# Kernel tuning notes

Hardware: AMD Instinct MI355X
Metric: run time of the kernel (lower is better)

The kernel has to match this reference:

```python
import jax, jax.numpy as jnp
import numpy as np

B, S, HID = 2, 2048, 2048
H, KV, D, E = 16, 4, 128, 32
NB = 9  # num_behavior + 1
EPS = 1e-6
SCALING = (E + D) ** -0.5


def rmsnorm(x, w, eps=EPS):
    # normalize over last dim in fp32, like Qwen3MoeRMSNorm
    xf = x.astype(jnp.float32)
    var = jnp.mean(xf * xf, axis=-1, keepdims=True)
    return (xf * jax.lax.rsqrt(var + eps)).astype(x.dtype) * w


def setup_inputs() -> dict:
    key = jax.random.key(0)
    ks = jax.random.split(key, 12)
    s = lambda n: 1.0 / np.sqrt(n)
    return {
        "hidden_states": jax.random.normal(ks[0], (B, S, HID), jnp.float32),
        "behavior_index": jax.random.randint(ks[1], (B, S), 0, NB),
        "q_proj_w": jax.random.normal(ks[2], (H * D, HID), jnp.float32) * s(HID),
        "k_proj_w": jax.random.normal(ks[3], (KV * D, HID), jnp.float32) * s(HID),
        "v_proj_w": jax.random.normal(ks[4], (KV * D, HID), jnp.float32) * s(HID),
        "o_proj_w": jax.random.normal(ks[5], (HID, H * D), jnp.float32) * s(H * D),
        "q_norm_w": jnp.ones((D,), jnp.float32),
        "k_norm_w": jnp.ones((D,), jnp.float32),
        "qbe_table": jax.random.normal(ks[6], (NB, H * E), jnp.float32),
        "kbe_table": jax.random.normal(ks[7], (NB, KV * E), jnp.float32),
        "qbn_w": jnp.ones((E,), jnp.float32),
        "kbn_w": jnp.ones((E,), jnp.float32),
    }


def reference(hidden_states, behavior_index, q_proj_w, k_proj_w, v_proj_w,
              o_proj_w, q_norm_w, k_norm_w, qbe_table, kbe_table, qbn_w, kbn_w):
    b, s, _ = hidden_states.shape
    # QKV projections + per-head RMSNorm on q/k
    q = rmsnorm((hidden_states @ q_proj_w.T).reshape(b, s, H, D), q_norm_w)
    k = rmsnorm((hidden_states @ k_proj_w.T).reshape(b, s, KV, D), k_norm_w)
    v = (hidden_states @ v_proj_w.T).reshape(b, s, KV, D)
    q = q.transpose(0, 2, 1, 3)  # [b,H,s,D]
    k = k.transpose(0, 2, 1, 3)  # [b,KV,s,D]
    v = v.transpose(0, 2, 1, 3)  # [b,KV,s,D]
    # behavior embeddings: lookup -> per-head RMSNorm -> concat onto head_dim
    qbe = rmsnorm(qbe_table[behavior_index].reshape(b, s, H, E), qbn_w).transpose(0, 2, 1, 3)
    kbe = rmsnorm(kbe_table[behavior_index].reshape(b, s, KV, E), kbn_w).transpose(0, 2, 1, 3)
    q = jnp.concatenate([q, qbe], axis=-1)  # [b,H,s,D+E]
    k = jnp.concatenate([k, kbe], axis=-1)  # [b,KV,s,D+E]
    # GQA: repeat kv heads
    g = H // KV
    k = jnp.repeat(k, g, axis=1)
    v = jnp.repeat(v, g, axis=1)
    # eager attention, causal, softmax in fp32
    scores = jnp.einsum('bhqd,bhkd->bhqk', q, k) * SCALING
    causal = jnp.tril(jnp.ones((s, s), bool))
    scores = jnp.where(causal, scores, jnp.finfo(scores.dtype).min)
    attn = jax.nn.softmax(scores.astype(jnp.float32), axis=-1).astype(q.dtype)
    out = jnp.einsum('bhqk,bhkd->bhqd', attn, v)  # [b,H,s,D]
    out = out.transpose(0, 2, 1, 3).reshape(b, s, H * D)
    return out @ o_proj_w.T
```

## Files before the change

### kernel.cpp

```cpp
#include <hip/hip_runtime.h>

typedef unsigned short u16;
typedef unsigned int u32;
typedef __bf16 bf16x8 __attribute__((ext_vector_type(8)));
typedef __bf16 b16x4 __attribute__((ext_vector_type(4)));
typedef short s16x4 __attribute__((ext_vector_type(4)));
typedef float f32x4 __attribute__((ext_vector_type(4)));

#define SCALE 0.07905694150420949f

__device__ __forceinline__ float bf2f(u16 h) { return __uint_as_float(((u32)h) << 16); }
__device__ __forceinline__ u16 f2bf(float f) {
  u32 u = __float_as_uint(f);
  u += 0x7fffu + ((u >> 16) & 1u);
  return (u16)(u >> 16);
}
__device__ __forceinline__ u16 f2bf_fast(float f) {
  return (u16)((__float_as_uint(f) + 0x8000u) >> 16);
}
__device__ __forceinline__ bf16x8 ldfrag(const u16* p) {
  int4 t = *reinterpret_cast<const int4*>(p);
  return __builtin_bit_cast(bf16x8, t);
}

__device__ __forceinline__ f32x4 mfma16x16(s16x4 a, s16x4 b, f32x4 c) {
#if __has_builtin(__builtin_amdgcn_mfma_f32_16x16x16bf16_1k)
  return __builtin_amdgcn_mfma_f32_16x16x16bf16_1k(a, b, c, 0, 0, 0);
#elif __has_builtin(__builtin_amdgcn_mfma_f32_16x16x16_bf16)
  return __builtin_amdgcn_mfma_f32_16x16x16_bf16(__builtin_bit_cast(b16x4, a),
                                                 __builtin_bit_cast(b16x4, b), c, 0, 0, 0);
#else
  asm volatile("s_nop 2\n\tv_mfma_f32_16x16x16_bf16 %0, %1, %2, %0"
               : "+v"(c) : "v"(a), "v"(b));
  return c;
#endif
}

__device__ __forceinline__ void gld16(const u16* g, u16* l) {
  __builtin_amdgcn_global_load_lds((const __attribute__((address_space(1))) u32*)(const void*)g,
                                   (__attribute__((address_space(3))) u32*)(void*)l, 16, 0, 0);
}

__global__ void conv_f32_bf16(const float* __restrict__ in, u16* __restrict__ out, int n) {
  int n4 = n >> 2;
  for (int i = blockIdx.x * blockDim.x + threadIdx.x; i < n4; i += gridDim.x * blockDim.x) {
    float4 v = reinterpret_cast<const float4*>(in)[i];
    ushort4 o = {f2bf(v.x), f2bf(v.y), f2bf(v.z), f2bf(v.w)};
    reinterpret_cast<ushort4*>(out)[i] = o;
  }
}

template <int OUT_BF16>
__global__ __launch_bounds__(256, 2) void gemm_bt(const u16* __restrict__ A,
                                                  const u16* __restrict__ Bw,
                                                  void* __restrict__ Cv,
                                                  int M, int N, int K) {
  __shared__ __align__(16) u16 As[2][8192];
  __shared__ __align__(16) u16 Bs[2][8192];
  const int tid = threadIdx.x;
  const int nbn = N >> 7;
  const int cpx = gridDim.x >> 3;
  const int swz = (blockIdx.x & 7) * cpx + (blockIdx.x >> 3);
  const int bm = swz / nbn, bn = swz % nbn;
  const int row0 = bm << 7, col0 = bn << 7;
  const int lane = tid & 63, w = tid >> 6;
  const int lg = lane >> 4, lr = lane & 15;
  const int wr = w >> 1, wc = w & 1;
  const int nt = K >> 6;

  auto stage = [&](int slot, int t) {
    const size_t k0 = (size_t)t << 6;
#pragma unroll
    for (int it = 0; it < 4; ++it) {
      int G = it * 256 + tid;
      int r = G >> 3, p = G & 7;
      int gs = p ^ (r & 7);
      gld16(&A[(size_t)(row0 + r) * K + k0 + gs * 8], &As[slot][(size_t)G * 8]);
      gld16(&Bw[(size_t)(col0 + r) * K + k0 + gs * 8], &Bs[slot][(size_t)G * 8]);
    }
  };

  f32x4 acc[4][4] = {};
  stage(0, 0);
  __syncthreads();

  for (int t = 0; t < nt; ++t) {
    const int slot = t & 1;
    if (t + 1 < nt) stage(slot ^ 1, t + 1);
#pragma unroll
    for (int kk = 0; kk < 2; ++kk) {
      bf16x8 af[4], bv[4];
#pragma unroll
      for (int m = 0; m < 4; ++m) {
        int r = wr * 64 + m * 16 + lr;
        int g = (kk * 4 + lg) ^ (lr & 7);
        af[m] = ldfrag(&As[slot][r * 64 + g * 8]);
      }
#pragma unroll
      for (int n = 0; n < 4; ++n) {
        int r = wc * 64 + n * 16 + lr;
        int g = (kk * 4 + lg) ^ (lr & 7);
        bv[n] = ldfrag(&Bs[slot][r * 64 + g * 8]);
      }
#pragma unroll
      for (int m = 0; m < 4; ++m)
#pragma unroll
        for (int n = 0; n < 4; ++n)
          acc[m][n] = __builtin_amdgcn_mfma_f32_16x16x32_bf16(af[m], bv[n], acc[m][n], 0, 0, 0);
    }
    __syncthreads();
  }

#pragma unroll
  for (int m = 0; m < 4; ++m)
#pragma unroll
    for (int n = 0; n < 4; ++n)
#pragma unroll
      for (int r = 0; r < 4; ++r) {
        int row = row0 + wr * 64 + m * 16 + lg * 4 + r;
        int col = col0 + wc * 64 + n * 16 + lr;
        float v = acc[m][n][r];
        if (OUT_BF16)
          ((u16*)Cv)[(size_t)row * N + col] = f2bf(v);
        else
          ((float*)Cv)[(size_t)row * N + col] = v;
      }
}

__global__ __launch_bounds__(256) void postproc(
    const u16* __restrict__ qkv, const int* __restrict__ bidx,
    const float* __restrict__ qnw, const float* __restrict__ knw,
    const float* __restrict__ qbe_t, const float* __restrict__ kbe_t,
    const float* __restrict__ qbn, const float* __restrict__ kbn,
    u16* __restrict__ qcat, u16* __restrict__ kcat, u16* __restrict__ vt) {
  const int tok = blockIdx.x;
  const int b = tok >> 11, s = tok & 2047;
  const int w = threadIdx.x >> 6, lane = threadIdx.x & 63;
  const int idx = bidx[tok];
  const u16* base = qkv + (size_t)tok * 3072;

  for (int h = w; h < 16; h += 4) {
    float x0 = bf2f(base[h * 128 + 2 * lane]);
    float x1 = bf2f(base[h * 128 + 2 * lane + 1]);
    float ss = x0 * x0 + x1 * x1;
#pragma unroll
    for (int o = 32; o; o >>= 1) ss += __shfl_xor(ss, o);
    float rn = rsqrtf(ss * (1.f / 128.f) + 1e-6f) * SCALE;
    size_t ob = ((size_t)(b * 16 + h) * 2048 + s) * 160;
    qcat[ob + 2 * lane] = f2bf(x0 * rn * qnw[2 * lane]);
    qcat[ob + 2 * lane + 1] = f2bf(x1 * rn * qnw[2 * lane + 1]);
    if (lane < 32) {
      float e = qbe_t[idx * 512 + h * 32 + lane];
      float s2 = e * e;
#pragma unroll
      for (int o = 16; o; o >>= 1) s2 += __shfl_xor(s2, o);
      qcat[ob + 128 + lane] = f2bf(e * rsqrtf(s2 * (1.f / 32.f) + 1e-6f) * qbn[lane] * SCALE);
    }
  }
  {
    const int kv = w;
    float x0 = bf2f(base[2048 + kv * 128 + 2 * lane]);
    float x1 = bf2f(base[2048 + kv * 128 + 2 * lane + 1]);
    float ss = x0 * x0 + x1 * x1;
#pragma unroll
    for (int o = 32; o; o >>= 1) ss += __shfl_xor(ss, o);
    float rn = rsqrtf(ss * (1.f / 128.f) + 1e-6f);
    size_t ob = ((size_t)(b * 4 + kv) * 2048 + s) * 160;
    kcat[ob + 2 * lane] = f2bf(x0 * rn * knw[2 * lane]);
    kcat[ob + 2 * lane + 1] = f2bf(x1 * rn * knw[2 * lane + 1]);
    if (lane < 32) {
      float e = kbe_t[idx * 128 + kv * 32 + lane];
      float s2 = e * e;
#pragma unroll
      for (int o = 16; o; o >>= 1) s2 += __shfl_xor(s2, o);
      kcat[ob + 128 + lane] = f2bf(e * rsqrtf(s2 * (1.f / 32.f) + 1e-6f) * kbn[lane]);
    }
    size_t vb = (size_t)(b * 4 + kv) * 128 * 2048;
    vt[vb + (size_t)lane * 2048 + s] = base[2560 + kv * 128 + lane];
    vt[vb + (size_t)(lane + 64) * 2048 + s] = base[2560 + kv * 128 + 64 + lane];
  }
}

__global__ __launch_bounds__(256, 2) void attn(const u16* __restrict__ qcat,
                                               const u16* __restrict__ kcat,
                                               const u16* __restrict__ vt,
                                               u16* __restrict__ aout) {
  __shared__ __align__(16) u16 Kls[2][10240];
  __shared__ __align__(16) u16 Vls[8192];
  const int tid = threadIdx.x;
  const int blk = blockIdx.x;
  const int kvh = blk & 3;
  const int b = (blk >> 2) & 1;
  const int hq = (blk >> 3) & 3;
  const int g = blk >> 5;
  const int h = kvh * 4 + hq;
  const int w = tid >> 6;
  const int lane = tid & 63;
  const int lg = lane >> 4, lr = lane & 15;
  const int qb_a = g * 4 + w;
  const int qb_b = 127 - qb_a;
  const int qpa = qb_a * 16 + lr;
  const int qpb = qb_b * 16 + lr;
  const int nt = 32 - g;

  const u16* qpA = qcat + ((size_t)(b * 16 + h) * 2048 + qb_a * 16) * 160;
  const u16* qpB = qcat + ((size_t)(b * 16 + h) * 2048 + qb_b * 16) * 160;
  bf16x8 qfa[5], qfb[5];
#pragma unroll
  for (int c = 0; c < 5; ++c) {
    qfa[c] = ldfrag(qpA + lr * 160 + c * 32 + lg * 8);
    qfb[c] = ldfrag(qpB + lr * 160 + c * 32 + lg * 8);
  }

  const u16* kbp = kcat + (size_t)(b * 4 + kvh) * 2048 * 160;
  const u16* vbp = vt + (size_t)(b * 4 + kvh) * 128 * 2048;

  auto stageK = [&](int buf, int kt) {
    const u16* ksrc = kbp + (size_t)kt * (64 * 160);
#pragma unroll
    for (int it = 0; it < 5; ++it) {
      int G = it * 256 + tid;
      int r = G / 20, p = G - r * 20;
      int gs = p ^ ((r >> 1) & 3);
      gld16(ksrc + r * 160 + gs * 8, &Kls[buf][G * 8]);
    }
  };
  auto stageV = [&](int kt) {
    const u16* vsrc = vbp + kt * 64;
#pragma unroll
    for (int it = 0; it < 4; ++it) {
      int G = it * 256 + tid;
      int r = G >> 3, p = G & 7;
      int gs = p ^ (r & 7);
      gld16(vsrc + (size_t)r * 2048 + gs * 8, &Vls[G * 8]);
    }
  };

  float ma = -INFINITY, la = 0.f, mb = -INFINITY, lb = 0.f;
  f32x4 acc_a[8] = {}, acc_b[8] = {};

  stageK(0, 0);
  stageV(0);
  __syncthreads();

  for (int kt = 0; kt < nt; ++kt) {
    const int buf = kt & 1;
    const bool aact = (kt <= g);
    if (kt + 1 < nt) stageK(buf ^ 1, kt + 1);

    f32x4 sa[4] = {}, sb[4] = {};
#pragma unroll
    for (int c = 0; c < 5; ++c) {
      bf16x8 kf[4];
#pragma unroll
      for (int i = 0; i < 4; ++i) {
        int r = i * 16 + lr;
        int p = (c * 4 + lg) ^ ((r >> 1) & 3);
        kf[i] = ldfrag(&Kls[buf][(r * 20 + p) * 8]);
      }
#pragma unroll
      for (int i = 0; i < 4; ++i)
        sb[i] = __builtin_amdgcn_mfma_f32_16x16x32_bf16(kf[i], qfb[c], sb[i], 0, 0, 0);
      if (aact)
#pragma unroll
        for (int i = 0; i < 4; ++i)
          sa[i] = __builtin_amdgcn_mfma_f32_16x16x32_bf16(kf[i], qfa[c], sa[i], 0, 0, 0);
    }

    s16x4 pka[4], pkb[4];
    auto soft = [&](f32x4 (&st)[4], float& mm, float& ls, f32x4 (&ac)[8], s16x4 (&pk)[4],
                    bool masked, int qpos) {
      float vmax = -INFINITY;
#pragma unroll
      for (int i = 0; i < 4; ++i)
#pragma unroll
        for (int r = 0; r < 4; ++r) {
          float v = st[i][r];
          if (masked && (kt * 64 + i * 16 + 4 * lg + r > qpos)) v = -INFINITY;
          st[i][r] = v;
          vmax = fmaxf(vmax, v);
        }
      vmax = fmaxf(vmax, __shfl_xor(vmax, 16));
      vmax = fmaxf(vmax, __shfl_xor(vmax, 32));
      bool skip = __all(vmax <= mm);
      float mn = skip ? mm : fmaxf(mm, vmax);
      float rs = 0.f;
#pragma unroll
      for (int i = 0; i < 4; ++i)
#pragma unroll
        for (int r = 0; r < 4; ++r) {
          float p = __expf(st[i][r] - mn);
          st[i][r] = p;
          rs += p;
        }
      rs += __shfl_xor(rs, 16);
      rs += __shfl_xor(rs, 32);
      if (skip) {
        ls += rs;
      } else {
        float corr = __expf(mm - mn);
        ls = ls * corr + rs;
        mm = mn;
        float c4[4];
#pragma unroll
        for (int r = 0; r < 4; ++r) c4[r] = __shfl(corr, 4 * lg + r);
#pragma unroll
        for (int dt = 0; dt < 8; ++dt)
#pragma unroll
          for (int r = 0; r < 4; ++r) ac[dt][r] *= c4[r];
      }
#pragma unroll
      for (int i = 0; i < 4; ++i) {
        pk[i][0] = (short)f2bf_fast(st[i][0]);
        pk[i][1] = (short)f2bf_fast(st[i][1]);
        pk[i][2] = (short)f2bf_fast(st[i][2]);
        pk[i][3] = (short)f2bf_fast(st[i][3]);
      }
    };
    soft(sb, mb, lb, acc_b, pkb, kt == nt - 1, qpb);
    if (aact) soft(sa, ma, la, acc_a, pka, kt == g, qpa);

    __syncthreads();

#pragma unroll
    for (int ks = 0; ks < 4; ++ks) {
      s16x4 vf[8];
#pragma unroll
      for (int dt = 0; dt < 8; ++dt) {
        int r = dt * 16 + lr;
        int p = (ks * 2 + (lg >> 1)) ^ (r & 7);
        vf[dt] = *reinterpret_cast<const s16x4*>(&Vls[(r * 8 + p) * 8 + (lg & 1) * 4]);
      }
#pragma unroll
      for (int dt = 0; dt < 8; ++dt) acc_b[dt] = mfma16x16(pkb[ks], vf[dt], acc_b[dt]);
      if (aact)
#pragma unroll
        for (int dt = 0; dt < 8; ++dt) acc_a[dt] = mfma16x16(pka[ks], vf[dt], acc_a[dt]);
    }

    __syncthreads();
    if (kt + 1 < nt) stageV(kt + 1);
  }

  float inva[4], invb[4];
#pragma unroll
  for (int r = 0; r < 4; ++r) {
    inva[r] = 1.f / __shfl(la, 4 * lg + r);
    invb[r] = 1.f / __shfl(lb, 4 * lg + r);
  }
#pragma unroll
  for (int dt = 0; dt < 8; ++dt)
#pragma unroll
    for (int r = 0; r < 4; ++r) {
      int rowa = qb_a * 16 + 4 * lg + r;
      int rowb = qb_b * 16 + 4 * lg + r;
      aout[((size_t)(b * 2048 + rowa) * 16 + h) * 128 + dt * 16 + lr] =
          f2bf(acc_a[dt][r] * inva[r]);
      aout[((size_t)(b * 2048 + rowb) * 16 + h) * 128 + dt * 16 + lr] =
          f2bf(acc_b[dt][r] * invb[r]);
    }
}

extern "C" void kernel_launch(void* const* d_in, const int* in_sizes, int n_in,
                              void* d_out, int out_size, void* d_ws, size_t ws_size,
                              hipStream_t stream) {
  const float* hs = (const float*)d_in[0];
  const int* bidx = (const int*)d_in[1];
  const float* qw = (const float*)d_in[2];
  const float* kw = (const float*)d_in[3];
  const float* vw = (const float*)d_in[4];
  const float* ow = (const float*)d_in[5];
  const float* qnw = (const float*)d_in[6];
  const float* knw = (const float*)d_in[7];
  const float* qbe_t = (const float*)d_in[8];
  const float* kbe_t = (const float*)d_in[9];
  const float* qbn = (const float*)d_in[10];
  const float* kbn = (const float*)d_in[11];

  u16* ws = (u16*)d_ws;
  u16* hs_bf = ws;
  u16* wqkv = hs_bf + 8388608;
  u16* ow_bf = wqkv + 6291456;
  u16* qkv = ow_bf + 4194304;
  u16* qcat = qkv + 12582912;
  u16* kcat = qcat + 10485760;
  u16* vt = kcat + 2621440;
  u16* attn_o = vt + 2097152;

  conv_f32_bf16<<<2048, 256, 0, stream>>>(hs, hs_bf, 8388608);
  conv_f32_bf16<<<1024, 256, 0, stream>>>(qw, wqkv, 4194304);
  conv_f32_bf16<<<512, 256, 0, stream>>>(kw, wqkv + 4194304, 1048576);
  conv_f32_bf16<<<512, 256, 0, stream>>>(vw, wqkv + 5242880, 1048576);
  conv_f32_bf16<<<1024, 256, 0, stream>>>(ow, ow_bf, 4194304);

  gemm_bt<1><<<dim3((4096 / 128) * (3072 / 128)), 256, 0, stream>>>(
      hs_bf, wqkv, (void*)qkv, 4096, 3072, 2048);

  postproc<<<4096, 256, 0, stream>>>(qkv, bidx, qnw, knw, qbe_t, kbe_t, qbn, kbn,
                                     qcat, kcat, vt);

  attn<<<512, 256, 0, stream>>>(qcat, kcat, vt, attn_o);

  gemm_bt<0><<<dim3((4096 / 128) * (2048 / 128)), 256, 0, stream>>>(
      attn_o, ow_bf, (void*)d_out, 4096, 2048, 2048);
}
```

Baseline: 229.8 us.

## Use exp2 softmax, lazy rescale, packed bf16 convert, setprio and new K swizzle

```diff
diff --git a/kernel.cpp b/kernel.cpp
--- a/kernel.cpp
+++ b/kernel.cpp
@@ -8,15 +8,13 @@
 typedef float f32x4 __attribute__((ext_vector_type(4)));
 
 #define SCALE 0.07905694150420949f
+#define LOG2E 1.4426950408889634f
 
 __device__ __forceinline__ float bf2f(u16 h) { return __uint_as_float(((u32)h) << 16); }
 __device__ __forceinline__ u16 f2bf(float f) {
   u32 u = __float_as_uint(f);
   u += 0x7fffu + ((u >> 16) & 1u);
   return (u16)(u >> 16);
-}
-__device__ __forceinline__ u16 f2bf_fast(float f) {
-  return (u16)((__float_as_uint(f) + 0x8000u) >> 16);
 }
 __device__ __forceinline__ bf16x8 ldfrag(const u16* p) {
   int4 t = *reinterpret_cast<const int4*>(p);
@@ -39,6 +37,12 @@
 __device__ __forceinline__ void gld16(const u16* g, u16* l) {
   __builtin_amdgcn_global_load_lds((const __attribute__((address_space(1))) u32*)(const void*)g,
                                    (__attribute__((address_space(3))) u32*)(void*)l, 16, 0, 0);
+}
+
+__device__ __forceinline__ u32 cvtpk(float s0, float s1) {
+  u32 w;
+  asm("v_cvt_pk_bf16_f32 %0, %1, %2" : "=v"(w) : "v"(s0), "v"(s1));
+  return w;
 }
 
 __global__ void conv_f32_bf16(const float* __restrict__ in, u16* __restrict__ out, int n) {
@@ -138,6 +142,7 @@
   const int w = threadIdx.x >> 6, lane = threadIdx.x & 63;
   const int idx = bidx[tok];
   const u16* base = qkv + (size_t)tok * 3072;
+  const float QS = SCALE * LOG2E;
 
   for (int h = w; h < 16; h += 4) {
     float x0 = bf2f(base[h * 128 + 2 * lane]);
@@ -145,7 +150,7 @@
     float ss = x0 * x0 + x1 * x1;
 #pragma unroll
     for (int o = 32; o; o >>= 1) ss += __shfl_xor(ss, o);
-    float rn = rsqrtf(ss * (1.f / 128.f) + 1e-6f) * SCALE;
+    float rn = rsqrtf(ss * (1.f / 128.f) + 1e-6f) * QS;
     size_t ob = ((size_t)(b * 16 + h) * 2048 + s) * 160;
     qcat[ob + 2 * lane] = f2bf(x0 * rn * qnw[2 * lane]);
     qcat[ob + 2 * lane + 1] = f2bf(x1 * rn * qnw[2 * lane + 1]);
@@ -154,7 +159,7 @@
       float s2 = e * e;
 #pragma unroll
       for (int o = 16; o; o >>= 1) s2 += __shfl_xor(s2, o);
-      qcat[ob + 128 + lane] = f2bf(e * rsqrtf(s2 * (1.f / 32.f) + 1e-6f) * qbn[lane] * SCALE);
+      qcat[ob + 128 + lane] = f2bf(e * rsqrtf(s2 * (1.f / 32.f) + 1e-6f) * qbn[lane] * QS);
     }
   }
   {
@@ -180,6 +185,8 @@
     vt[vb + (size_t)(lane + 64) * 2048 + s] = base[2560 + kv * 128 + 64 + lane];
   }
 }
+
+__device__ __forceinline__ int kswz(int r) { return ((r >> 1) & 3) ^ ((r >> 3) & 1); }
 
 __global__ __launch_bounds__(256, 2) void attn(const u16* __restrict__ qcat,
                                                const u16* __restrict__ kcat,
@@ -221,7 +228,7 @@
     for (int it = 0; it < 5; ++it) {
       int G = it * 256 + tid;
       int r = G / 20, p = G - r * 20;
-      int gs = p ^ ((r >> 1) & 3);
+      int gs = p ^ kswz(r);
       gld16(ksrc + r * 160 + gs * 8, &Kls[buf][G * 8]);
     }
   };
@@ -249,13 +256,14 @@
     if (kt + 1 < nt) stageK(buf ^ 1, kt + 1);
 
     f32x4 sa[4] = {}, sb[4] = {};
+    __builtin_amdgcn_s_setprio(1);
 #pragma unroll
     for (int c = 0; c < 5; ++c) {
       bf16x8 kf[4];
 #pragma unroll
       for (int i = 0; i < 4; ++i) {
         int r = i * 16 + lr;
-        int p = (c * 4 + lg) ^ ((r >> 1) & 3);
+        int p = (c * 4 + lg) ^ kswz(r);
         kf[i] = ldfrag(&Kls[buf][(r * 20 + p) * 8]);
       }
 #pragma unroll
@@ -266,6 +274,7 @@
         for (int i = 0; i < 4; ++i)
           sa[i] = __builtin_amdgcn_mfma_f32_16x16x32_bf16(kf[i], qfa[c], sa[i], 0, 0, 0);
     }
+    __builtin_amdgcn_s_setprio(0);
 
     s16x4 pka[4], pkb[4];
     auto soft = [&](f32x4 (&st)[4], float& mm, float& ls, f32x4 (&ac)[8], s16x4 (&pk)[4],
@@ -282,14 +291,14 @@
         }
       vmax = fmaxf(vmax, __shfl_xor(vmax, 16));
       vmax = fmaxf(vmax, __shfl_xor(vmax, 32));
-      bool skip = __all(vmax <= mm);
+      bool skip = __all(vmax <= mm + 8.f);
       float mn = skip ? mm : fmaxf(mm, vmax);
       float rs = 0.f;
 #pragma unroll
       for (int i = 0; i < 4; ++i)
 #pragma unroll
         for (int r = 0; r < 4; ++r) {
-          float p = __expf(st[i][r] - mn);
+          float p = exp2f(st[i][r] - mn);
           st[i][r] = p;
           rs += p;
         }
@@ -298,7 +307,7 @@
       if (skip) {
         ls += rs;
       } else {
-        float corr = __expf(mm - mn);
+        float corr = exp2f(mm - mn);
         ls = ls * corr + rs;
         mm = mn;
         float c4[4];
@@ -311,10 +320,8 @@
       }
 #pragma unroll
       for (int i = 0; i < 4; ++i) {
-        pk[i][0] = (short)f2bf_fast(st[i][0]);
-        pk[i][1] = (short)f2bf_fast(st[i][1]);
-        pk[i][2] = (short)f2bf_fast(st[i][2]);
-        pk[i][3] = (short)f2bf_fast(st[i][3]);
+        uint2 ww = {cvtpk(st[i][0], st[i][1]), cvtpk(st[i][2], st[i][3])};
+        pk[i] = __builtin_bit_cast(s16x4, ww);
       }
     };
     soft(sb, mb, lb, acc_b, pkb, kt == nt - 1, qpb);
@@ -322,6 +329,7 @@
 
     __syncthreads();
 
+    __builtin_amdgcn_s_setprio(1);
 #pragma unroll
     for (int ks = 0; ks < 4; ++ks) {
       s16x4 vf[8];
@@ -337,6 +345,7 @@
 #pragma unroll
         for (int dt = 0; dt < 8; ++dt) acc_a[dt] = mfma16x16(pka[ks], vf[dt], acc_a[dt]);
     }
+    __builtin_amdgcn_s_setprio(0);
 
     __syncthreads();
     if (kt + 1 < nt) stageV(kt + 1);
```

New measurement: 254.1 us. +10.6%, slower.
